# Optimization experiments

Measured on AMD Instinct MI355X. Metric: run time of the kernel, lower is better.

## Reference

```python
import jax, jax.numpy as jnp
import numpy as np

EMB = 128
N_RBF = 16
N_EDGES = 1_000_000
N_ATOMS = 50_000


def setup_inputs() -> dict:
    key = jax.random.key(0)
    ks = jax.random.split(key, 16)
    inp = {
        "x": jax.random.normal(ks[0], (N_EDGES, EMB), dtype=jnp.float32),
        "rbf": jax.random.normal(ks[1], (N_EDGES, N_RBF), dtype=jnp.float32),
        "idnb_i": jax.random.randint(ks[2], (N_EDGES,), 0, N_ATOMS, dtype=jnp.int32),
        "n_atoms": N_ATOMS,
        # learned params
        "W_x": jax.random.normal(ks[3], (EMB, EMB), dtype=jnp.float32) * 0.05,
        "b_x": jnp.zeros((EMB,), dtype=jnp.float32),
        "W_rbf": jax.random.normal(ks[4], (N_RBF, EMB), dtype=jnp.float32) * 0.2,
        "b_rbf": jnp.zeros((EMB,), dtype=jnp.float32),
        "W1": jax.random.normal(ks[5], (EMB, EMB), dtype=jnp.float32) * 0.05,
        "b1": jnp.zeros((EMB,), dtype=jnp.float32),
        "W2": jax.random.normal(ks[6], (EMB, EMB), dtype=jnp.float32) * 0.05,
        "b2": jnp.zeros((EMB,), dtype=jnp.float32),
        "W3": jax.random.normal(ks[7], (EMB, EMB), dtype=jnp.float32) * 0.05,
        "b3": jnp.zeros((EMB,), dtype=jnp.float32),
        "W_final": jax.random.normal(ks[8], (EMB, 1), dtype=jnp.float32) * 0.05,
        # scale coefficients (shape [1] as in the keras layer)
        "coef_rbf_a": jnp.exp(jax.random.normal(ks[9], (1,)) * 0.01),
        "coef_rbf_b": jnp.exp(jax.random.normal(ks[10], (1,)) * 0.01),
        "coef_x": jnp.exp(jax.random.normal(ks[11], (1,)) * 0.01),
        "coef_final": jnp.exp(jax.random.normal(ks[12], (1,)) * 0.01),
    }
    return inp


def reference(x, rbf, idnb_i, n_atoms, W_x, b_x, W_rbf, b_rbf, W1, b1, W2, b2,
              W3, b3, W_final, coef_rbf_a, coef_rbf_b, coef_x, coef_final):
    act = jax.nn.silu  # keras 'swish'
    rbf = coef_rbf_a * rbf
    h = act(x @ W_x + b_x)                      # [E, emb]
    g = act(rbf @ W_rbf + b_rbf)                # [E, emb]
    conv_x = (coef_rbf_b * g) * (coef_x * h)    # fused elementwise gate
    a = jax.ops.segment_sum(conv_x, idnb_i, num_segments=n_atoms)  # [n_atoms, emb]
    a = act(a @ W1 + b1)
    a = act(a @ W2 + b2)
    a = act(a @ W3 + b3)
    out = (a @ W_final) * coef_final            # [n_atoms, 1]
    return out
```

## Files before the change

### kernel.cpp

```cpp
#include <hip/hip_runtime.h>

#define E_TOTAL 1000000
#define EMB     128
#define NRBF    16
#define NATOMS  50000
#define APB     40
#define NBLK    ((NATOMS + 255) / 256)

typedef _Float16 f16x8 __attribute__((ext_vector_type(8)));
typedef _Float16 f16x4 __attribute__((ext_vector_type(4)));
typedef float    f32x4 __attribute__((ext_vector_type(4)));

__device__ __forceinline__ float silu_f(float v) {
    return v * (1.0f / (1.0f + __expf(-v)));
}

__device__ __forceinline__ int sigma64(int e) {
    return (((e & 15) >> 2) << 4) + ((e >> 4) << 2) + (e & 3);
}

__global__ __launch_bounds__(256)
void hist_kernel(const int* __restrict__ idnb, int* __restrict__ counts) {
    const int e = blockIdx.x * 256 + threadIdx.x;
    if (e < E_TOTAL) atomicAdd(&counts[idnb[e]], 1);
}

__global__ __launch_bounds__(256)
void scan1_kernel(const int* __restrict__ counts, int* __restrict__ row_ptr,
                  int* __restrict__ bsums) {
    __shared__ int sd[256];
    const int tid = threadIdx.x;
    const int idx = blockIdx.x * 256 + tid;
    const int v = (idx < NATOMS) ? counts[idx] : 0;
    sd[tid] = v;
    __syncthreads();
#pragma unroll
    for (int off = 1; off < 256; off <<= 1) {
        const int t = (tid >= off) ? sd[tid - off] : 0;
        __syncthreads();
        sd[tid] += t;
        __syncthreads();
    }
    if (idx < NATOMS) row_ptr[idx] = sd[tid] - v;
    if (tid == 255) bsums[blockIdx.x] = sd[255];
}

__global__ __launch_bounds__(256)
void scan2_kernel(int* __restrict__ bsums) {
    __shared__ int sd[256];
    const int tid = threadIdx.x;
    const int v = (tid < NBLK) ? bsums[tid] : 0;
    sd[tid] = v;
    __syncthreads();
#pragma unroll
    for (int off = 1; off < 256; off <<= 1) {
        const int t = (tid >= off) ? sd[tid - off] : 0;
        __syncthreads();
        sd[tid] += t;
        __syncthreads();
    }
    if (tid < NBLK) bsums[tid] = sd[tid] - v;
}

__global__ __launch_bounds__(256)
void scan3_kernel(const int* __restrict__ bsums, int* __restrict__ row_ptr,
                  int* __restrict__ cursor) {
    const int idx = blockIdx.x * 256 + threadIdx.x;
    if (idx < NATOMS) {
        const int r = row_ptr[idx] + bsums[blockIdx.x];
        row_ptr[idx] = r;
        cursor[idx]  = r;
    }
    if (idx == 0) row_ptr[NATOMS] = E_TOTAL;
}

__global__ __launch_bounds__(256)
void scatter_kernel(const int* __restrict__ idnb, int* __restrict__ cursor,
                    int* __restrict__ eidx) {
    const int e = blockIdx.x * 256 + threadIdx.x;
    if (e < E_TOTAL) {
        const int a = idnb[e];
        const int p = atomicAdd(&cursor[a], 1);
        eidx[p] = e;
    }
}

__global__ __launch_bounds__(256, 2)
void edge_kernel(const float* __restrict__ x,
                 const float* __restrict__ rbf,
                 const int*   __restrict__ eidx,
                 const int*   __restrict__ row_ptr,
                 const float* __restrict__ Wx,
                 const float* __restrict__ bx,
                 const float* __restrict__ Wr,
                 const float* __restrict__ br,
                 const float* __restrict__ c_a,
                 const float* __restrict__ c_b,
                 const float* __restrict__ c_x,
                 float* __restrict__ acc)
{
    __shared__ _Float16 sX[64 * 128];
    __shared__ _Float16 sR[64 * 40];
    __shared__ float    sAcc[APB][132];
    __shared__ int      sAid[64];

    const int tid  = threadIdx.x;
    const int w    = tid >> 6;
    const int lane = tid & 63;
    const int lq   = lane >> 4;
    const int lm   = lane & 15;

    const int aBase = blockIdx.x * APB;

    int rp[APB];
#pragma unroll
    for (int a = 0; a < APB; ++a) rp[a] = row_ptr[aBase + a];
    const int eBeg = rp[0];
    const int eEnd = row_ptr[aBase + APB];
    const int nEdge = eEnd - eBeg;
    const int ntile = (nEdge + 63) >> 6;

    const float ca = c_a[0];
    const float sc = c_b[0] * c_x[0];
    const int col0 = w * 32 + lm;
    const int col1 = col0 + 16;
    const float bx0 = bx[col0], bx1 = bx[col1];
    const float br0 = br[col0], br1 = br[col1];

    f16x8 wxh[4][2], wxl[4][2], wrh[2];
#pragma unroll
    for (int ks = 0; ks < 4; ++ks)
#pragma unroll
        for (int nt = 0; nt < 2; ++nt) {
            const int n = w * 32 + nt * 16 + lm;
            f16x8 h8, l8;
#pragma unroll
            for (int j = 0; j < 8; ++j) {
                const int k = ks * 32 + lq * 8 + j;
                const float v = Wx[k * EMB + n];
                const _Float16 hv = (_Float16)v;
                h8[j] = hv;
                l8[j] = (_Float16)(v - (float)hv);
            }
            wxh[ks][nt] = h8;
            wxl[ks][nt] = l8;
        }
#pragma unroll
    for (int nt = 0; nt < 2; ++nt) {
        const int n = w * 32 + nt * 16 + lm;
        f16x8 h8;
#pragma unroll
        for (int j = 0; j < 8; ++j) {
            const int k = lq * 8 + j;
            h8[j] = (_Float16)((k < NRBF) ? Wr[k * EMB + n] : 0.f);
        }
        wrh[nt] = h8;
    }

    for (int f = tid; f < APB * 132; f += 256) ((float*)sAcc)[f] = 0.f;
    for (int f = tid; f < 64 * 24; f += 256)
        sR[(f / 24) * 40 + 16 + (f % 24)] = (_Float16)0.f;

    float4 px[8];
    float4 pr;
    int    prel = -1;

    auto prefetch = [&](int t) {
        const int nb = eBeg + t * 64;
#pragma unroll
        for (int i = 0; i < 8; ++i) {
            const int e = (tid >> 5) + i * 8;
            const int eid = eidx[min(nb + sigma64(e), eEnd - 1)];
            px[i] = *(const float4*)(x + (size_t)eid * EMB + (tid & 31) * 4);
        }
        {
            const int er = tid >> 2;
            const int eid = eidx[min(nb + sigma64(er), eEnd - 1)];
            pr = *(const float4*)(rbf + (size_t)eid * NRBF + (tid & 3) * 4);
        }
        if (tid < 64) {
            const int pos = nb + tid;
            if (pos >= eEnd) {
                prel = -1;
            } else {
                int rel = 0;
#pragma unroll
                for (int a = 1; a < APB; ++a) rel += (pos >= rp[a]) ? 1 : 0;
                prel = rel;
            }
        }
    };

    auto write_lds = [&]() {
#pragma unroll
        for (int i = 0; i < 8; ++i) {
            const int e = (tid >> 5) + i * 8;
            const int kb = (tid & 31) * 4;
            const int idx = (e * 128 + kb) ^ ((e & 7) << 3);
            f16x4 h4 = {(_Float16)px[i].x, (_Float16)px[i].y,
                        (_Float16)px[i].z, (_Float16)px[i].w};
            *(f16x4*)&sX[idx] = h4;
        }
        {
            const int er = tid >> 2;
            const int kb = (tid & 3) * 4;
            f16x4 r4 = {(_Float16)(pr.x * ca), (_Float16)(pr.y * ca),
                        (_Float16)(pr.z * ca), (_Float16)(pr.w * ca)};
            *(f16x4*)&sR[er * 40 + kb] = r4;
        }
        if (tid < 64) sAid[tid] = prel;
    };

    if (ntile > 0) prefetch(0);

    for (int t = 0; t < ntile; ++t) {
        __syncthreads();
        write_lds();
        __syncthreads();
        if (t + 1 < ntile) prefetch(t + 1);

        int   curA = -2;
        float a0v = 0.f, a1v = 0.f;

        auto epi = [&](const f32x4 hac[2], const f32x4 gac[2], int mt) {
            const int pbase = lq * 16 + mt * 4;
            float v0[4], v1[4];
#pragma unroll
            for (int r = 0; r < 4; ++r) {
                const float g0 = gac[0][r] + br0, h0 = hac[0][r] + bx0;
                const float g1 = gac[1][r] + br1, h1 = hac[1][r] + bx1;
                const float d0 = (1.f + __expf(-g0)) * (1.f + __expf(-h0));
                const float d1 = (1.f + __expf(-g1)) * (1.f + __expf(-h1));
                v0[r] = sc * g0 * h0 * __builtin_amdgcn_rcpf(d0);
                v1[r] = sc * g1 * h1 * __builtin_amdgcn_rcpf(d1);
            }
#pragma unroll
            for (int r = 0; r < 4; ++r) {
                const int rel = sAid[pbase + r];
                if (rel != curA) {
                    if (curA >= 0) {
                        atomicAdd(&sAcc[curA][col0], a0v);
                        atomicAdd(&sAcc[curA][col1], a1v);
                    }
                    curA = rel; a0v = 0.f; a1v = 0.f;
                }
                a0v += v0[r];
                a1v += v1[r];
            }
        };

        auto mfma_mt = [&](f32x4 hac[2], f32x4 gac[2], int mt) {
#pragma unroll
            for (int nt = 0; nt < 2; ++nt) { hac[nt] = 0.f; gac[nt] = 0.f; }
            const int m = mt * 16 + lm;
            const f16x8 rh = *(const f16x8*)&sR[m * 40 + lq * 8];
#pragma unroll
            for (int nt = 0; nt < 2; ++nt)
                gac[nt] = __builtin_amdgcn_mfma_f32_16x16x32_f16(rh, wrh[nt], gac[nt], 0, 0, 0);
#pragma unroll
            for (int ks = 0; ks < 4; ++ks) {
                const int xi = (m * 128 + ks * 32 + lq * 8) ^ ((m & 7) << 3);
                const f16x8 xh = *(const f16x8*)&sX[xi];
#pragma unroll
                for (int nt = 0; nt < 2; ++nt) {
                    hac[nt] = __builtin_amdgcn_mfma_f32_16x16x32_f16(xh, wxh[ks][nt], hac[nt], 0, 0, 0);
                    hac[nt] = __builtin_amdgcn_mfma_f32_16x16x32_f16(xh, wxl[ks][nt], hac[nt], 0, 0, 0);
                }
            }
        };

#pragma unroll
        for (int g = 0; g < 2; ++g) {
            f32x4 hacA[2], gacA[2], hacB[2], gacB[2];
            mfma_mt(hacA, gacA, g * 2);
            mfma_mt(hacB, gacB, g * 2 + 1);
            epi(hacA, gacA, g * 2);
            epi(hacB, gacB, g * 2 + 1);
        }

        if (curA >= 0) {
            atomicAdd(&sAcc[curA][col0], a0v);
            atomicAdd(&sAcc[curA][col1], a1v);
        }
    }

    __syncthreads();
#pragma unroll
    for (int it = 0; it < 3; ++it) {
        const int r = (tid >> 4) + it * 16;
        if (r < APB) {
            const int c = (tid & 15) * 8;
            float* dst = acc + (size_t)(aBase + r) * EMB + c;
            *(float4*)(dst)     = *(const float4*)&sAcc[r][c];
            *(float4*)(dst + 4) = *(const float4*)&sAcc[r][c + 4];
        }
    }
}

__global__ __launch_bounds__(256, 2)
void mlp_fused_kernel(const float* __restrict__ X,
                      const float* __restrict__ W1, const float* __restrict__ b1,
                      const float* __restrict__ W2, const float* __restrict__ b2,
                      const float* __restrict__ W3, const float* __restrict__ b3,
                      const float* __restrict__ Wf, const float* __restrict__ cf,
                      float* __restrict__ out, int M)
{
    __shared__ _Float16 sA[128 * 128];
    __shared__ _Float16 sB[128 * 128];
    __shared__ float    sOut[128];

    const int tid  = threadIdx.x;
    const int w    = tid >> 6;
    const int lane = tid & 63;
    const int lq   = lane >> 4;
    const int lm   = lane & 15;

    const int base = blockIdx.x * 128;
    const int col0 = w * 32 + lm;
    const int col1 = col0 + 16;
    const float wf0 = Wf[col0], wf1 = Wf[col1];
    const float cfv = cf[0];

    if (tid < 128) sOut[tid] = 0.f;

#pragma unroll
    for (int i = 0; i < 16; ++i) {
        const int e = (tid >> 5) + i * 8;
        const int row = min(base + e, M - 1);
        const float4 v = *(const float4*)(X + (size_t)row * EMB + (tid & 31) * 4);
        const int kb = (tid & 31) * 4;
        const int idx = (e * 128 + kb) ^ ((e & 7) << 3);
        f16x4 h4 = {(_Float16)v.x, (_Float16)v.y, (_Float16)v.z, (_Float16)v.w};
        *(f16x4*)&sA[idx] = h4;
    }
    __syncthreads();

    const float* Ws[3] = {W1, W2, W3};
    const float* bs[3] = {b1, b2, b3};

#pragma unroll 1
    for (int L = 0; L < 3; ++L) {
        const _Float16* sIn   = (L & 1) ? sB : sA;
        _Float16*       sDst  = (L & 1) ? sA : sB;
        const float*    W     = Ws[L];
        const float     bb0   = bs[L][col0];
        const float     bb1   = bs[L][col1];

        f16x8 wh[4][2], wl[4][2];
#pragma unroll
        for (int ks = 0; ks < 4; ++ks)
#pragma unroll
            for (int nt = 0; nt < 2; ++nt) {
                const int n = w * 32 + nt * 16 + lm;
                f16x8 h8, l8;
#pragma unroll
                for (int j = 0; j < 8; ++j) {
                    const int k = ks * 32 + lq * 8 + j;
                    const float v = W[k * EMB + n];
                    const _Float16 hv = (_Float16)v;
                    h8[j] = hv;
                    l8[j] = (_Float16)(v - (float)hv);
                }
                wh[ks][nt] = h8;
                wl[ks][nt] = l8;
            }

#pragma unroll
        for (int sub = 0; sub < 2; ++sub) {
#pragma unroll
            for (int mth = 0; mth < 2; ++mth) {
                f32x4 hac[2][2];
#pragma unroll
                for (int mi = 0; mi < 2; ++mi)
#pragma unroll
                    for (int nt = 0; nt < 2; ++nt) hac[mi][nt] = 0.f;

#pragma unroll
                for (int mi = 0; mi < 2; ++mi) {
                    const int m = sub * 64 + (mth * 2 + mi) * 16 + lm;
#pragma unroll
                    for (int ks = 0; ks < 4; ++ks) {
                        const int xi = (m * 128 + ks * 32 + lq * 8) ^ ((m & 7) << 3);
                        const f16x8 xh = *(const f16x8*)&sIn[xi];
#pragma unroll
                        for (int nt = 0; nt < 2; ++nt) {
                            hac[mi][nt] = __builtin_amdgcn_mfma_f32_16x16x32_f16(xh, wh[ks][nt], hac[mi][nt], 0, 0, 0);
                            hac[mi][nt] = __builtin_amdgcn_mfma_f32_16x16x32_f16(xh, wl[ks][nt], hac[mi][nt], 0, 0, 0);
                        }
                    }
                }

#pragma unroll
                for (int mi = 0; mi < 2; ++mi) {
                    const int rowl = sub * 64 + (mth * 2 + mi) * 16 + lq * 4;
                    if (L < 2) {
#pragma unroll
                        for (int r = 0; r < 4; ++r) {
                            const float o0 = silu_f(hac[mi][0][r] + bb0);
                            const float o1 = silu_f(hac[mi][1][r] + bb1);
                            const int rw = rowl + r;
                            sDst[(rw * 128 + col0) ^ ((rw & 7) << 3)] = (_Float16)o0;
                            sDst[(rw * 128 + col1) ^ ((rw & 7) << 3)] = (_Float16)o1;
                        }
                    } else {
#pragma unroll
                        for (int r = 0; r < 4; ++r) {
                            const float o0 = silu_f(hac[mi][0][r] + bb0);
                            const float o1 = silu_f(hac[mi][1][r] + bb1);
                            float p = o0 * wf0 + o1 * wf1;
#pragma unroll
                            for (int off = 1; off < 16; off <<= 1)
                                p += __shfl_xor(p, off);
                            if (lm == 0 && base + rowl + r < M)
                                atomicAdd(&sOut[rowl + r], p);
                        }
                    }
                }
            }
        }
        __syncthreads();
    }

    if (tid < 128) {
        const int row = base + tid;
        if (row < M) out[row] = sOut[tid] * cfv;
    }
}

extern "C" void kernel_launch(void* const* d_in, const int* in_sizes, int n_in,
                              void* d_out, int out_size, void* d_ws, size_t ws_size,
                              hipStream_t stream) {
    const float* x    = (const float*)d_in[0];
    const float* rbf  = (const float*)d_in[1];
    const int*   idnb = (const int*)  d_in[2];
    const float* Wx   = (const float*)d_in[4];
    const float* bx   = (const float*)d_in[5];
    const float* Wr   = (const float*)d_in[6];
    const float* brf  = (const float*)d_in[7];
    const float* W1   = (const float*)d_in[8];
    const float* b1   = (const float*)d_in[9];
    const float* W2   = (const float*)d_in[10];
    const float* b2   = (const float*)d_in[11];
    const float* W3   = (const float*)d_in[12];
    const float* b3   = (const float*)d_in[13];
    const float* Wf   = (const float*)d_in[14];
    const float* c_a  = (const float*)d_in[15];
    const float* c_b  = (const float*)d_in[16];
    const float* c_x  = (const float*)d_in[17];
    const float* c_f  = (const float*)d_in[18];

    float* out = (float*)d_out;
    float* acc = (float*)d_ws;
    float* buf = acc + (size_t)NATOMS * EMB;
    int* eidx    = (int*)buf;
    int* counts  = eidx + E_TOTAL;
    int* row_ptr = counts + NATOMS;
    int* cursor  = row_ptr + NATOMS + 1;
    int* bsums   = cursor + NATOMS;

    hipMemsetAsync(counts, 0, NATOMS * sizeof(int), stream);

    hist_kernel<<<(E_TOTAL + 255) / 256, 256, 0, stream>>>(idnb, counts);
    scan1_kernel<<<NBLK, 256, 0, stream>>>(counts, row_ptr, bsums);
    scan2_kernel<<<1, 256, 0, stream>>>(bsums);
    scan3_kernel<<<NBLK, 256, 0, stream>>>(bsums, row_ptr, cursor);
    scatter_kernel<<<(E_TOTAL + 255) / 256, 256, 0, stream>>>(idnb, cursor, eidx);

    edge_kernel<<<NATOMS / APB, 256, 0, stream>>>(x, rbf, eidx, row_ptr,
                                                  Wx, bx, Wr, brf,
                                                  c_a, c_b, c_x, acc);

    mlp_fused_kernel<<<(NATOMS + 127) / 128, 256, 0, stream>>>(
        acc, W1, b1, W2, b2, W3, b3, Wf, c_f, out, NATOMS);
}
```

Measured before the change: 379.1 us.

## Split edge kernel columns across eight waves with 512-thread blocks

Doubles the edge kernel's block to 512 threads (8 waves), so each wave computes 16 output columns instead of 32. This halves per-thread weight registers, accumulators and MFMA work, and the prefetch and writeback loops are redistributed over the larger block. The aim is more latency hiding and memory parallelism per block. In exchange, each wave does less MFMA work per LDS tile, every wave issues more shared-memory atomics, and the larger blocks may lower occupancy.

```diff
diff --git a/kernel.cpp b/kernel.cpp
--- a/kernel.cpp
+++ b/kernel.cpp
@@ -85,7 +85,7 @@
     }
 }
 
-__global__ __launch_bounds__(256, 2)
+__global__ __launch_bounds__(512, 1)
 void edge_kernel(const float* __restrict__ x,
                  const float* __restrict__ rbf,
                  const int*   __restrict__ eidx,
@@ -122,58 +122,52 @@
 
     const float ca = c_a[0];
     const float sc = c_b[0] * c_x[0];
-    const int col0 = w * 32 + lm;
-    const int col1 = col0 + 16;
-    const float bx0 = bx[col0], bx1 = bx[col1];
-    const float br0 = br[col0], br1 = br[col1];
-
-    f16x8 wxh[4][2], wxl[4][2], wrh[2];
-#pragma unroll
-    for (int ks = 0; ks < 4; ++ks)
-#pragma unroll
-        for (int nt = 0; nt < 2; ++nt) {
-            const int n = w * 32 + nt * 16 + lm;
-            f16x8 h8, l8;
-#pragma unroll
-            for (int j = 0; j < 8; ++j) {
-                const int k = ks * 32 + lq * 8 + j;
-                const float v = Wx[k * EMB + n];
-                const _Float16 hv = (_Float16)v;
-                h8[j] = hv;
-                l8[j] = (_Float16)(v - (float)hv);
-            }
-            wxh[ks][nt] = h8;
-            wxl[ks][nt] = l8;
-        }
-#pragma unroll
-    for (int nt = 0; nt < 2; ++nt) {
-        const int n = w * 32 + nt * 16 + lm;
+    const int col0 = w * 16 + lm;
+    const float bx0 = bx[col0];
+    const float br0 = br[col0];
+
+    f16x8 wxh[4], wxl[4], wrh;
+#pragma unroll
+    for (int ks = 0; ks < 4; ++ks) {
+        f16x8 h8, l8;
+#pragma unroll
+        for (int j = 0; j < 8; ++j) {
+            const int k = ks * 32 + lq * 8 + j;
+            const float v = Wx[k * EMB + col0];
+            const _Float16 hv = (_Float16)v;
+            h8[j] = hv;
+            l8[j] = (_Float16)(v - (float)hv);
+        }
+        wxh[ks] = h8;
+        wxl[ks] = l8;
+    }
+    {
         f16x8 h8;
 #pragma unroll
         for (int j = 0; j < 8; ++j) {
             const int k = lq * 8 + j;
-            h8[j] = (_Float16)((k < NRBF) ? Wr[k * EMB + n] : 0.f);
-        }
-        wrh[nt] = h8;
-    }
-
-    for (int f = tid; f < APB * 132; f += 256) ((float*)sAcc)[f] = 0.f;
-    for (int f = tid; f < 64 * 24; f += 256)
+            h8[j] = (_Float16)((k < NRBF) ? Wr[k * EMB + col0] : 0.f);
+        }
+        wrh = h8;
+    }
+
+    for (int f = tid; f < APB * 132; f += 512) ((float*)sAcc)[f] = 0.f;
+    for (int f = tid; f < 64 * 24; f += 512)
         sR[(f / 24) * 40 + 16 + (f % 24)] = (_Float16)0.f;
 
-    float4 px[8];
+    float4 px[4];
     float4 pr;
     int    prel = -1;
 
     auto prefetch = [&](int t) {
         const int nb = eBeg + t * 64;
 #pragma unroll
-        for (int i = 0; i < 8; ++i) {
-            const int e = (tid >> 5) + i * 8;
+        for (int i = 0; i < 4; ++i) {
+            const int e = (tid >> 5) + i * 16;
             const int eid = eidx[min(nb + sigma64(e), eEnd - 1)];
             px[i] = *(const float4*)(x + (size_t)eid * EMB + (tid & 31) * 4);
         }
-        {
+        if (tid < 256) {
             const int er = tid >> 2;
             const int eid = eidx[min(nb + sigma64(er), eEnd - 1)];
             pr = *(const float4*)(rbf + (size_t)eid * NRBF + (tid & 3) * 4);
@@ -193,15 +187,15 @@
 
     auto write_lds = [&]() {
 #pragma unroll
-        for (int i = 0; i < 8; ++i) {
-            const int e = (tid >> 5) + i * 8;
+        for (int i = 0; i < 4; ++i) {
+            const int e = (tid >> 5) + i * 16;
             const int kb = (tid & 31) * 4;
             const int idx = (e * 128 + kb) ^ ((e & 7) << 3);
             f16x4 h4 = {(_Float16)px[i].x, (_Float16)px[i].y,
                         (_Float16)px[i].z, (_Float16)px[i].w};
             *(f16x4*)&sX[idx] = h4;
         }
-        {
+        if (tid < 256) {
             const int er = tid >> 2;
             const int kb = (tid & 3) * 4;
             f16x4 r4 = {(_Float16)(pr.x * ca), (_Float16)(pr.y * ca),
@@ -220,74 +214,59 @@
         if (t + 1 < ntile) prefetch(t + 1);
 
         int   curA = -2;
-        float a0v = 0.f, a1v = 0.f;
-
-        auto epi = [&](const f32x4 hac[2], const f32x4 gac[2], int mt) {
+        float a0v = 0.f;
+
+        auto epi = [&](const f32x4& hac, const f32x4& gac, int mt) {
             const int pbase = lq * 16 + mt * 4;
-            float v0[4], v1[4];
+            float v0[4];
 #pragma unroll
             for (int r = 0; r < 4; ++r) {
-                const float g0 = gac[0][r] + br0, h0 = hac[0][r] + bx0;
-                const float g1 = gac[1][r] + br1, h1 = hac[1][r] + bx1;
+                const float g0 = gac[r] + br0, h0 = hac[r] + bx0;
                 const float d0 = (1.f + __expf(-g0)) * (1.f + __expf(-h0));
-                const float d1 = (1.f + __expf(-g1)) * (1.f + __expf(-h1));
                 v0[r] = sc * g0 * h0 * __builtin_amdgcn_rcpf(d0);
-                v1[r] = sc * g1 * h1 * __builtin_amdgcn_rcpf(d1);
             }
 #pragma unroll
             for (int r = 0; r < 4; ++r) {
                 const int rel = sAid[pbase + r];
                 if (rel != curA) {
-                    if (curA >= 0) {
-                        atomicAdd(&sAcc[curA][col0], a0v);
-                        atomicAdd(&sAcc[curA][col1], a1v);
-                    }
-                    curA = rel; a0v = 0.f; a1v = 0.f;
+                    if (curA >= 0) atomicAdd(&sAcc[curA][col0], a0v);
+                    curA = rel; a0v = 0.f;
                 }
                 a0v += v0[r];
-                a1v += v1[r];
             }
         };
 
-        auto mfma_mt = [&](f32x4 hac[2], f32x4 gac[2], int mt) {
-#pragma unroll
-            for (int nt = 0; nt < 2; ++nt) { hac[nt] = 0.f; gac[nt] = 0.f; }
+        auto mfma_mt = [&](f32x4& hac, f32x4& gac, int mt) {
+            hac = 0.f; gac = 0.f;
             const int m = mt * 16 + lm;
             const f16x8 rh = *(const f16x8*)&sR[m * 40 + lq * 8];
-#pragma unroll
-            for (int nt = 0; nt < 2; ++nt)
-                gac[nt] = __builtin_amdgcn_mfma_f32_16x16x32_f16(rh, wrh[nt], gac[nt], 0, 0, 0);
+            gac = __builtin_amdgcn_mfma_f32_16x16x32_f16(rh, wrh, gac, 0, 0, 0);
 #pragma unroll
             for (int ks = 0; ks < 4; ++ks) {
                 const int xi = (m * 128 + ks * 32 + lq * 8) ^ ((m & 7) << 3);
                 const f16x8 xh = *(const f16x8*)&sX[xi];
-#pragma unroll
-                for (int nt = 0; nt < 2; ++nt) {
-                    hac[nt] = __builtin_amdgcn_mfma_f32_16x16x32_f16(xh, wxh[ks][nt], hac[nt], 0, 0, 0);
-                    hac[nt] = __builtin_amdgcn_mfma_f32_16x16x32_f16(xh, wxl[ks][nt], hac[nt], 0, 0, 0);
-                }
+                hac = __builtin_amdgcn_mfma_f32_16x16x32_f16(xh, wxh[ks], hac, 0, 0, 0);
+                hac = __builtin_amdgcn_mfma_f32_16x16x32_f16(xh, wxl[ks], hac, 0, 0, 0);
             }
         };
 
 #pragma unroll
         for (int g = 0; g < 2; ++g) {
-            f32x4 hacA[2], gacA[2], hacB[2], gacB[2];
+            f32x4 hacA, gacA, hacB, gacB;
             mfma_mt(hacA, gacA, g * 2);
             mfma_mt(hacB, gacB, g * 2 + 1);
             epi(hacA, gacA, g * 2);
             epi(hacB, gacB, g * 2 + 1);
         }
 
-        if (curA >= 0) {
+        if (curA >= 0)
             atomicAdd(&sAcc[curA][col0], a0v);
-            atomicAdd(&sAcc[curA][col1], a1v);
-        }
     }
 
     __syncthreads();
 #pragma unroll
-    for (int it = 0; it < 3; ++it) {
-        const int r = (tid >> 4) + it * 16;
+    for (int it = 0; it < 2; ++it) {
+        const int r = (tid >> 4) + it * 32;
         if (r < APB) {
             const int c = (tid & 15) * 8;
             float* dst = acc + (size_t)(aBase + r) * EMB + c;
@@ -466,7 +445,7 @@
     scan3_kernel<<<NBLK, 256, 0, stream>>>(bsums, row_ptr, cursor);
     scatter_kernel<<<(E_TOTAL + 255) / 256, 256, 0, stream>>>(idnb, cursor, eidx);
 
-    edge_kernel<<<NATOMS / APB, 256, 0, stream>>>(x, rbf, eidx, row_ptr,
+    edge_kernel<<<NATOMS / APB, 512, 0, stream>>>(x, rbf, eidx, row_ptr,
                                                   Wx, bx, Wr, brf,
                                                   c_a, c_b, c_x, acc);
 
```

New measurement: 383.4 us. About the same (+1.1%).
